# Kernel tuning notes

Measured on AMD Instinct MI355X. Metric: run time of the kernel, lower is better.

## Reference

```python
import jax, jax.numpy as jnp
import numpy as np

N = 20000
E = 320000
F_IN = 512
F_OUT = 512
DIFF_T = 1.0
NUM_STEPS = 5
TIME_DECAY = 0.1
LN_EPS = 1e-5


def setup_inputs() -> dict:
    key = jax.random.key(0)
    k_x, k_e, k_ts, k_wt, k_wr = jax.random.split(key, 5)
    x = jax.random.normal(k_x, (N, F_IN), dtype=jnp.float32)
    edge_index = jax.random.randint(k_e, (2, E), 0, N)
    timestamps = jax.random.uniform(k_ts, (E,), dtype=jnp.float32) * 100.0
    lim = float(np.sqrt(6.0 / (F_IN + F_OUT)))  # xavier_uniform
    W_t = jax.random.uniform(k_wt, (F_OUT, F_IN), jnp.float32, -lim, lim)
    b_t = jnp.zeros((F_OUT,), jnp.float32)
    W_r = jax.random.uniform(k_wr, (F_OUT, F_IN), jnp.float32, -lim, lim)
    gamma = jnp.ones((F_OUT,), jnp.float32)
    beta = jnp.zeros((F_OUT,), jnp.float32)
    return {"node_features": x, "edge_index": edge_index, "timestamps": timestamps,
            "W_t": W_t, "b_t": b_t, "W_r": W_r, "gamma": gamma, "beta": beta,
            "graph_time": 100}


def reference(node_features, edge_index, timestamps, W_t, b_t, W_r, gamma, beta, graph_time):
    x = node_features
    n = x.shape[0]
    # append self-loops with timestamp == graph.time
    loop = jnp.arange(n)
    ei = jnp.concatenate([edge_index, jnp.stack([loop, loop], axis=0)], axis=1)
    ts = jnp.concatenate([timestamps, jnp.full((n,), graph_time, jnp.float32)])
    src, dst = ei[0], ei[1]
    # time-decayed symmetric-normalized adjacency weights
    w = jnp.exp(-TIME_DECAY * (ts.max() - ts))  # [E+N]
    deg = jax.ops.segment_sum(w, dst, num_segments=n)  # [N]
    dinv = jnp.where(deg > 0, deg ** -0.5, 0.0)
    ew = dinv[src] * w * dinv[dst]  # [E+N]
    # K Euler steps of heat diffusion: h <- h + dt*(A_norm h - h)
    dt = DIFF_T / NUM_STEPS
    h = x
    for _ in range(NUM_STEPS):
        diffused = jax.ops.segment_sum(ew[:, None] * h[src], dst, num_segments=n)  # [N, F]
        h = h + dt * (diffused - h)
    # transform + residual + layernorm (dropout omitted: eval mode)
    out = jax.nn.relu(h @ W_t.T + b_t) + x @ W_r.T  # [N, F_OUT]
    mu = out.mean(axis=-1, keepdims=True)
    var = out.var(axis=-1, keepdims=True)
    out = (out - mu) * jax.lax.rsqrt(var + LN_EPS) * gamma + beta
    return out
```

## Files before the change

### kernel.cpp

```cpp
#include <hip/hip_runtime.h>
#include <hip/hip_fp16.h>

#define FDIM 512
#define TDK  0.1f
#define DTs  0.2f
#define EPSv 1e-5f

using bf16x8  = __attribute__((ext_vector_type(8))) __bf16;
using floatx4 = __attribute__((ext_vector_type(4))) float;
using ushort8 = __attribute__((ext_vector_type(8))) unsigned short;
using uintx4  = __attribute__((ext_vector_type(4))) unsigned int;

__device__ __forceinline__ unsigned short f2bf(float f) {
  unsigned int u = __float_as_uint(f);
  u += 0x7fffu + ((u >> 16) & 1u);
  return (unsigned short)(u >> 16);
}

__device__ __forceinline__ void gld16(const __bf16* g, __bf16* l) {
  __builtin_amdgcn_global_load_lds(
      (const __attribute__((address_space(1))) unsigned int*)g,
      (__attribute__((address_space(3))) unsigned int*)l, 16, 0, 0);
}

__global__ __launch_bounds__(256) void tsmax_kernel(const float* __restrict__ ts, int E,
                                                    float* __restrict__ out) {
  float m = 0.f;
  for (int i = blockIdx.x * blockDim.x + threadIdx.x; i < E; i += gridDim.x * blockDim.x)
    m = fmaxf(m, ts[i]);
  for (int off = 32; off; off >>= 1) m = fmaxf(m, __shfl_down(m, off));
  __shared__ float sm[4];
  int wid = threadIdx.x >> 6, lane = threadIdx.x & 63;
  if (lane == 0) sm[wid] = m;
  __syncthreads();
  if (threadIdx.x == 0) {
    float mm = fmaxf(fmaxf(sm[0], sm[1]), fmaxf(sm[2], sm[3]));
    atomicMax((int*)out, __float_as_int(mm));
  }
}

__global__ __launch_bounds__(256) void edge_w_deg(const int* __restrict__ src, const int* __restrict__ dst,
                                                  const float* __restrict__ ts, const float* __restrict__ tsmax_p,
                                                  const int* __restrict__ gt_p,
                                                  float* __restrict__ w, float* __restrict__ deg,
                                                  int* __restrict__ cnt, int E, int N) {
  int e = blockIdx.x * blockDim.x + threadIdx.x;
  int total = E + N;
  if (e >= total) return;
  float gtf = (float)(*gt_p);
  float tm = fmaxf(*tsmax_p, gtf);
  int d; float t;
  if (e < E) { d = dst[e]; t = ts[e]; }
  else       { d = e - E;  t = gtf; }
  float wv = expf(-TDK * (tm - t));
  w[e] = wv;
  atomicAdd(&deg[d], wv);
  atomicAdd(&cnt[d], 1);
}

__global__ __launch_bounds__(256) void dinv_kernel(const float* __restrict__ deg, float* __restrict__ dinv, int N) {
  int i = blockIdx.x * blockDim.x + threadIdx.x;
  if (i >= N) return;
  float d = deg[i];
  dinv[i] = (d > 0.f) ? rsqrtf(d) : 0.f;
}

__global__ __launch_bounds__(256) void seg_reduce(const int* __restrict__ cnt, int* __restrict__ bsum, int n) {
  int i = blockIdx.x * 256 + threadIdx.x;
  int v = (i < n) ? cnt[i] : 0;
  for (int o = 32; o; o >>= 1) v += __shfl_down(v, o);
  __shared__ int sm[4];
  if ((threadIdx.x & 63) == 0) sm[threadIdx.x >> 6] = v;
  __syncthreads();
  if (threadIdx.x == 0) bsum[blockIdx.x] = sm[0] + sm[1] + sm[2] + sm[3];
}

__global__ __launch_bounds__(256) void scan_bsum(const int* __restrict__ bsum, int* __restrict__ bbase, int nb) {
  __shared__ int sm[256];
  int t = threadIdx.x;
  int v = (t < nb) ? bsum[t] : 0;
  sm[t] = v;
  __syncthreads();
  for (int o = 1; o < 256; o <<= 1) {
    int u = (t >= o) ? sm[t - o] : 0;
    __syncthreads();
    sm[t] += u;
    __syncthreads();
  }
  if (t < nb) bbase[t] = sm[t] - v;
}

__global__ __launch_bounds__(256) void seg_scan(const int* __restrict__ cnt, const int* __restrict__ bbase,
                                                int* __restrict__ offs, int* __restrict__ cursor,
                                                int n, int totE) {
  __shared__ int sm[256];
  int i = blockIdx.x * 256 + threadIdx.x;
  int v = (i < n) ? cnt[i] : 0;
  sm[threadIdx.x] = v;
  __syncthreads();
  for (int o = 1; o < 256; o <<= 1) {
    int u = (threadIdx.x >= o) ? sm[threadIdx.x - o] : 0;
    __syncthreads();
    sm[threadIdx.x] += u;
    __syncthreads();
  }
  int excl = sm[threadIdx.x] - v + bbase[blockIdx.x];
  if (i < n) { offs[i] = excl; cursor[i] = excl; }
  if (i == 0) offs[n] = totE;
}

__global__ __launch_bounds__(256) void scatter_kernel(const int* __restrict__ src, const int* __restrict__ dst,
                                                      const float* __restrict__ w, const float* __restrict__ dinv,
                                                      int* __restrict__ cursor, unsigned* __restrict__ cv,
                                                      int E, int N) {
  int e = blockIdx.x * blockDim.x + threadIdx.x;
  if (e >= E + N) return;
  int s, d;
  if (e < E) { s = src[e]; d = dst[e]; }
  else       { s = d = e - E; }
  int pos = atomicAdd(&cursor[d], 1);
  float v = dinv[s] * w[e] * dinv[d];
  unsigned short hv = __half_as_ushort(__float2half(v));
  cv[pos] = (unsigned)s | ((unsigned)hv << 16);
}

__device__ __forceinline__ void acc8(uintx4 u, float v, float* a) {
  a[0] += v * __uint_as_float(u[0] << 16);
  a[1] += v * __uint_as_float(u[0] & 0xffff0000u);
  a[2] += v * __uint_as_float(u[1] << 16);
  a[3] += v * __uint_as_float(u[1] & 0xffff0000u);
  a[4] += v * __uint_as_float(u[2] << 16);
  a[5] += v * __uint_as_float(u[2] & 0xffff0000u);
  a[6] += v * __uint_as_float(u[3] << 16);
  a[7] += v * __uint_as_float(u[3] & 0xffff0000u);
}

__device__ __forceinline__ float cvval(unsigned cu) {
  return __half2float(__ushort_as_half((unsigned short)(cu >> 16)));
}

__global__ __launch_bounds__(256) void spmm_xcd(const int* __restrict__ offs, const unsigned* __restrict__ cv,
                                                const unsigned short* __restrict__ h_in,
                                                unsigned short* __restrict__ h_out, int N) {
  int chunk = blockIdx.x & 7;
  int tile  = blockIdx.x >> 3;
  int row = tile * 32 + (threadIdx.x >> 3);
  if (row >= N) return;
  int fo = chunk * 64 + (threadIdx.x & 7) * 8;
  const unsigned short* hp = h_in + fo;
  int s = offs[row], e = offs[row + 1];
  float a[8] = {0.f, 0.f, 0.f, 0.f, 0.f, 0.f, 0.f, 0.f};
  int j = s;
  for (; j + 8 <= e; j += 8) {
    unsigned cu[8]; uintx4 u[8];
#pragma unroll
    for (int t = 0; t < 8; ++t) cu[t] = cv[j + t];
#pragma unroll
    for (int t = 0; t < 8; ++t) u[t] = *(const uintx4*)(hp + ((cu[t] & 0xffffu) << 9));
#pragma unroll
    for (int t = 0; t < 8; ++t) acc8(u[t], cvval(cu[t]), a);
  }
  if (j + 4 <= e) {
    unsigned cu[4]; uintx4 u[4];
#pragma unroll
    for (int t = 0; t < 4; ++t) cu[t] = cv[j + t];
#pragma unroll
    for (int t = 0; t < 4; ++t) u[t] = *(const uintx4*)(hp + ((cu[t] & 0xffffu) << 9));
#pragma unroll
    for (int t = 0; t < 4; ++t) acc8(u[t], cvval(cu[t]), a);
    j += 4;
  }
  for (; j < e; ++j) {
    unsigned cu = cv[j];
    uintx4 u = *(const uintx4*)(hp + ((cu & 0xffffu) << 9));
    acc8(u, cvval(cu), a);
  }
  uintx4 ud = *(const uintx4*)(hp + (row << 9));
  float hd[8];
  hd[0] = __uint_as_float(ud[0] << 16); hd[1] = __uint_as_float(ud[0] & 0xffff0000u);
  hd[2] = __uint_as_float(ud[1] << 16); hd[3] = __uint_as_float(ud[1] & 0xffff0000u);
  hd[4] = __uint_as_float(ud[2] << 16); hd[5] = __uint_as_float(ud[2] & 0xffff0000u);
  hd[6] = __uint_as_float(ud[3] << 16); hd[7] = __uint_as_float(ud[3] & 0xffff0000u);
  uintx4 o;
  unsigned int p0, p1;
#define PACK(k0, k1, dst_)                                        \
  { float o0 = hd[k0] + DTs * (a[k0] - hd[k0]);                   \
    float o1 = hd[k1] + DTs * (a[k1] - hd[k1]);                   \
    p0 = f2bf(o0); p1 = f2bf(o1); dst_ = p0 | (p1 << 16); }
  PACK(0, 1, o[0]) PACK(2, 3, o[1]) PACK(4, 5, o[2]) PACK(6, 7, o[3])
#undef PACK
  __builtin_nontemporal_store(o, (uintx4*)(h_out + (size_t)row * FDIM + fo));
}

__global__ __launch_bounds__(256) void cast_bf16(const float* __restrict__ srcp,
                                                 unsigned short* __restrict__ dstp, int n8) {
  int i = blockIdx.x * blockDim.x + threadIdx.x;
  if (i >= n8) return;
  const float4 v0 = *(const float4*)(srcp + (size_t)i * 8);
  const float4 v1 = *(const float4*)(srcp + (size_t)i * 8 + 4);
  ushort8 o;
  o[0] = f2bf(v0.x); o[1] = f2bf(v0.y); o[2] = f2bf(v0.z); o[3] = f2bf(v0.w);
  o[4] = f2bf(v1.x); o[5] = f2bf(v1.y); o[6] = f2bf(v1.z); o[7] = f2bf(v1.w);
  *(ushort8*)(dstp + (size_t)i * 8) = o;
}

__global__ __launch_bounds__(256, 2) void gemm_fused(const __bf16* __restrict__ Ah, const __bf16* __restrict__ Ax,
                                                     const __bf16* __restrict__ Wt, const __bf16* __restrict__ Wr,
                                                     const float* __restrict__ bias, float* __restrict__ out,
                                                     int M) {
  __shared__ __bf16 sA1[2][128 * 32];
  __shared__ __bf16 sA2[2][128 * 32];
  __shared__ __bf16 sB1[2][128 * 32];
  __shared__ __bf16 sB2[2][128 * 32];
  int tid = threadIdx.x;
  int wid = tid >> 6, lane = tid & 63;
  int wm = wid & 1, wn = wid >> 1;
  int lane15 = lane & 15, quad = lane >> 4;
  int m0 = blockIdx.x * 128, n0 = blockIdx.y * 128;

  int r0 = wid * 32 + (lane >> 2);
  int c0 = ((((lane & 3) - (lane >> 3)) & 3)) * 8;
  int am0 = m0 + r0;      if (am0 >= M) am0 = M - 1;
  int am1 = m0 + r0 + 16; if (am1 >= M) am1 = M - 1;
  int bn0 = n0 + r0;
  const __bf16* gA1_0 = Ah + (size_t)am0 * FDIM + c0;
  const __bf16* gA1_1 = Ah + (size_t)am1 * FDIM + c0;
  const __bf16* gA2_0 = Ax + (size_t)am0 * FDIM + c0;
  const __bf16* gA2_1 = Ax + (size_t)am1 * FDIM + c0;
  const __bf16* gB1_0 = Wt + (size_t)bn0 * FDIM + c0;
  const __bf16* gB1_1 = Wt + (size_t)(bn0 + 16) * FDIM + c0;
  const __bf16* gB2_0 = Wr + (size_t)bn0 * FDIM + c0;
  const __bf16* gB2_1 = Wr + (size_t)(bn0 + 16) * FDIM + c0;
  int loff0 = wid * 1024;
  int loff1 = wid * 1024 + 512;

  auto stage = [&](int b, int kt) {
    gld16(gA1_0 + kt, &sA1[b][loff0]); gld16(gA1_1 + kt, &sA1[b][loff1]);
    gld16(gB1_0 + kt, &sB1[b][loff0]); gld16(gB1_1 + kt, &sB1[b][loff1]);
    gld16(gA2_0 + kt, &sA2[b][loff0]); gld16(gA2_1 + kt, &sA2[b][loff1]);
    gld16(gB2_0 + kt, &sB2[b][loff0]); gld16(gB2_1 + kt, &sB2[b][loff1]);
  };

  int koff = ((quad + (lane15 >> 1)) & 3) * 8;

  floatx4 acc1[4][4], acc2[4][4];
  floatx4 z4; z4[0] = 0.f; z4[1] = 0.f; z4[2] = 0.f; z4[3] = 0.f;
#pragma unroll
  for (int im = 0; im < 4; ++im)
#pragma unroll
    for (int in = 0; in < 4; ++in) { acc1[im][in] = z4; acc2[im][in] = z4; }

  stage(0, 0);
  for (int it = 0; it < 16; ++it) {
    int cb = it & 1;
    __syncthreads();
    if (it + 1 < 16) stage(1 - cb, (it + 1) * 32);
    bf16x8 af[4], br[4];
#pragma unroll
    for (int im = 0; im < 4; ++im)
      af[im] = *(const bf16x8*)(&sA1[cb][(wm * 64 + im * 16 + lane15) * 32 + koff]);
#pragma unroll
    for (int in = 0; in < 4; ++in)
      br[in] = *(const bf16x8*)(&sB1[cb][(wn * 64 + in * 16 + lane15) * 32 + koff]);
#pragma unroll
    for (int im = 0; im < 4; ++im)
#pragma unroll
      for (int in = 0; in < 4; ++in)
        acc1[im][in] = __builtin_amdgcn_mfma_f32_16x16x32_bf16(af[im], br[in], acc1[im][in], 0, 0, 0);
#pragma unroll
    for (int im = 0; im < 4; ++im)
      af[im] = *(const bf16x8*)(&sA2[cb][(wm * 64 + im * 16 + lane15) * 32 + koff]);
#pragma unroll
    for (int in = 0; in < 4; ++in)
      br[in] = *(const bf16x8*)(&sB2[cb][(wn * 64 + in * 16 + lane15) * 32 + koff]);
#pragma unroll
    for (int im = 0; im < 4; ++im)
#pragma unroll
      for (int in = 0; in < 4; ++in)
        acc2[im][in] = __builtin_amdgcn_mfma_f32_16x16x32_bf16(af[im], br[in], acc2[im][in], 0, 0, 0);
  }

  float bn[4];
#pragma unroll
  for (int in = 0; in < 4; ++in) bn[in] = bias[n0 + wn * 64 + in * 16 + lane15];
#pragma unroll
  for (int im = 0; im < 4; ++im) {
#pragma unroll
    for (int in = 0; in < 4; ++in) {
#pragma unroll
      for (int r = 0; r < 4; ++r) {
        int m = m0 + wm * 64 + im * 16 + quad * 4 + r;
        int n = n0 + wn * 64 + in * 16 + lane15;
        if (m < M) {
          float v = fmaxf(acc1[im][in][r] + bn[in], 0.f) + acc2[im][in][r];
          out[(size_t)m * FDIM + n] = v;
        }
      }
    }
  }
}

__global__ __launch_bounds__(256) void ln_kernel(const float* __restrict__ pre, const float* __restrict__ gamma,
                                                 const float* __restrict__ beta, float* __restrict__ out) {
  int row = blockIdx.x, t = threadIdx.x;
  float2 v = *(const float2*)(pre + (size_t)row * FDIM + t * 2);
  float s = v.x + v.y;
  float ss = v.x * v.x + v.y * v.y;
  for (int off = 32; off; off >>= 1) { s += __shfl_down(s, off); ss += __shfl_down(ss, off); }
  __shared__ float sm[4], sm2[4];
  int wid = t >> 6, lane = t & 63;
  if (lane == 0) { sm[wid] = s; sm2[wid] = ss; }
  __syncthreads();
  if (t == 0) {
    float a = sm[0] + sm[1] + sm[2] + sm[3];
    float b = sm2[0] + sm2[1] + sm2[2] + sm2[3];
    sm[0] = a; sm2[0] = b;
  }
  __syncthreads();
  float mu = sm[0] * (1.f / FDIM);
  float var = sm2[0] * (1.f / FDIM) - mu * mu;
  float inv = rsqrtf(var + EPSv);
  float2 g  = *(const float2*)(gamma + t * 2);
  float2 bb = *(const float2*)(beta + t * 2);
  float2 o;
  o.x = (v.x - mu) * inv * g.x + bb.x;
  o.y = (v.y - mu) * inv * g.y + bb.y;
  *(float2*)(out + (size_t)row * FDIM + t * 2) = o;
}

extern "C" void kernel_launch(void* const* d_in, const int* in_sizes, int n_in,
                              void* d_out, int out_size, void* d_ws, size_t ws_size,
                              hipStream_t stream) {
  const float* x     = (const float*)d_in[0];
  const int*   ei    = (const int*)d_in[1];
  const float* ts    = (const float*)d_in[2];
  const float* W_t   = (const float*)d_in[3];
  const float* b_t   = (const float*)d_in[4];
  const float* W_r   = (const float*)d_in[5];
  const float* gamma = (const float*)d_in[6];
  const float* beta  = (const float*)d_in[7];
  const int*   gt    = (const int*)d_in[8];

  const int E = in_sizes[2];
  const int N = in_sizes[0] / FDIM;
  const int* src = ei;
  const int* dst = ei + E;
  const int totE = E + N;
  const int nb = (N + 255) / 256;

  char* base = (char*)d_ws;
  size_t off = 0;
  auto carve = [&](size_t bytes) -> char* {
    char* r = base + off;
    off = (off + bytes + 255) & ~(size_t)255;
    return r;
  };
  float* tsmax = (float*)carve(4);
  float* deg   = (float*)carve((size_t)N * 4);
  int*   cnt   = (int*)  carve((size_t)N * 4);
  size_t zero_bytes = off;
  float* dinv  = (float*)carve((size_t)N * 4);
  int*   offs  = (int*)  carve((size_t)(N + 1) * 4);
  int*   cursor= (int*)  carve((size_t)N * 4);
  int*   bsum  = (int*)  carve((size_t)nb * 4);
  int*   bbase = (int*)  carve((size_t)nb * 4);
  float* w     = (float*)carve((size_t)totE * 4);
  unsigned* cv = (unsigned*)carve((size_t)totE * 4);
  unsigned short* xb  = (unsigned short*)carve((size_t)N * FDIM * 2);
  unsigned short* hba = (unsigned short*)carve((size_t)N * FDIM * 2);
  unsigned short* hbb = (unsigned short*)carve((size_t)N * FDIM * 2);
  unsigned short* wtb = (unsigned short*)carve((size_t)FDIM * FDIM * 2);
  unsigned short* wrb = (unsigned short*)carve((size_t)FDIM * FDIM * 2);
  float* preLN = (float*)carve((size_t)N * FDIM * 4);

  hipMemsetAsync(d_ws, 0, zero_bytes, stream);

  tsmax_kernel<<<64, 256, 0, stream>>>(ts, E, tsmax);
  edge_w_deg<<<(totE + 255) / 256, 256, 0, stream>>>(src, dst, ts, tsmax, gt, w, deg, cnt, E, N);
  dinv_kernel<<<(N + 255) / 256, 256, 0, stream>>>(deg, dinv, N);
  seg_reduce<<<nb, 256, 0, stream>>>(cnt, bsum, N);
  scan_bsum<<<1, 256, 0, stream>>>(bsum, bbase, nb);
  seg_scan<<<nb, 256, 0, stream>>>(cnt, bbase, offs, cursor, N, totE);
  scatter_kernel<<<(totE + 255) / 256, 256, 0, stream>>>(src, dst, w, dinv, cursor, cv, E, N);

  int n8x = N * FDIM / 8;
  cast_bf16<<<(n8x + 255) / 256, 256, 0, stream>>>(x, xb, n8x);
  int n8w = FDIM * FDIM / 8;
  cast_bf16<<<(n8w + 255) / 256, 256, 0, stream>>>(W_t, wtb, n8w);
  cast_bf16<<<(n8w + 255) / 256, 256, 0, stream>>>(W_r, wrb, n8w);

  int sgrid = ((N + 31) / 32) * 8;
  spmm_xcd<<<sgrid, 256, 0, stream>>>(offs, cv, xb,  hba, N);
  spmm_xcd<<<sgrid, 256, 0, stream>>>(offs, cv, hba, hbb, N);
  spmm_xcd<<<sgrid, 256, 0, stream>>>(offs, cv, hbb, hba, N);
  spmm_xcd<<<sgrid, 256, 0, stream>>>(offs, cv, hba, hbb, N);
  spmm_xcd<<<sgrid, 256, 0, stream>>>(offs, cv, hbb, hba, N);

  dim3 gg((N + 127) / 128, FDIM / 128);
  gemm_fused<<<gg, 256, 0, stream>>>((const __bf16*)hba, (const __bf16*)xb,
                                     (const __bf16*)wtb, (const __bf16*)wrb,
                                     b_t, preLN, N);

  ln_kernel<<<N, 256, 0, stream>>>(preLN, gamma, beta, (float*)d_out);
}
```

Baseline: 403.1 us.

## Serialize dual GEMM into one accumulator and remap blocks per XCD

The fused GEMM now computes relu(h·W_tᵀ+b) first into a single accumulator set over 16 k-steps, applies bias and ReLU in place, then keeps accumulating x·W_rᵀ over another 16 steps. This halves the accumulator registers and the shared-memory tiles so three blocks per CU can fit. Block indices are also remapped to a 1D grid so that consecutive tiles land on the same XCD, improving L2 reuse of A rows. The cost is a serialized 32-step loop with the same MFMA count and one extra branch per iteration.

```diff
diff --git a/kernel.cpp b/kernel.cpp
--- a/kernel.cpp
+++ b/kernel.cpp
@@ -204,97 +204,100 @@
   *(ushort8*)(dstp + (size_t)i * 8) = o;
 }
 
-__global__ __launch_bounds__(256, 2) void gemm_fused(const __bf16* __restrict__ Ah, const __bf16* __restrict__ Ax,
+__global__ __launch_bounds__(256, 3) void gemm_fused(const __bf16* __restrict__ Ah, const __bf16* __restrict__ Ax,
                                                      const __bf16* __restrict__ Wt, const __bf16* __restrict__ Wr,
                                                      const float* __restrict__ bias, float* __restrict__ out,
-                                                     int M) {
-  __shared__ __bf16 sA1[2][128 * 32];
-  __shared__ __bf16 sA2[2][128 * 32];
-  __shared__ __bf16 sB1[2][128 * 32];
-  __shared__ __bf16 sB2[2][128 * 32];
+                                                     int M, int NB) {
+  __shared__ __bf16 sA[2][128 * 32];
+  __shared__ __bf16 sB[2][128 * 32];
   int tid = threadIdx.x;
   int wid = tid >> 6, lane = tid & 63;
   int wm = wid & 1, wn = wid >> 1;
   int lane15 = lane & 15, quad = lane >> 4;
-  int m0 = blockIdx.x * 128, n0 = blockIdx.y * 128;
+
+  int d = blockIdx.x;
+  int x = d & 7, s = d >> 3;
+  int q = NB >> 3, r = NB & 7;
+  int g = (x < r ? x * (q + 1) : r * (q + 1) + (x - r) * q) + s;
+  int mi = g >> 2, ni = g & 3;
+  int m0 = mi * 128, n0 = ni * 128;
 
   int r0 = wid * 32 + (lane >> 2);
   int c0 = ((((lane & 3) - (lane >> 3)) & 3)) * 8;
   int am0 = m0 + r0;      if (am0 >= M) am0 = M - 1;
   int am1 = m0 + r0 + 16; if (am1 >= M) am1 = M - 1;
   int bn0 = n0 + r0;
-  const __bf16* gA1_0 = Ah + (size_t)am0 * FDIM + c0;
-  const __bf16* gA1_1 = Ah + (size_t)am1 * FDIM + c0;
-  const __bf16* gA2_0 = Ax + (size_t)am0 * FDIM + c0;
-  const __bf16* gA2_1 = Ax + (size_t)am1 * FDIM + c0;
-  const __bf16* gB1_0 = Wt + (size_t)bn0 * FDIM + c0;
-  const __bf16* gB1_1 = Wt + (size_t)(bn0 + 16) * FDIM + c0;
-  const __bf16* gB2_0 = Wr + (size_t)bn0 * FDIM + c0;
-  const __bf16* gB2_1 = Wr + (size_t)(bn0 + 16) * FDIM + c0;
+  const __bf16* a00 = Ah + (size_t)am0 * FDIM + c0;
+  const __bf16* a01 = Ah + (size_t)am1 * FDIM + c0;
+  const __bf16* a10 = Ax + (size_t)am0 * FDIM + c0;
+  const __bf16* a11 = Ax + (size_t)am1 * FDIM + c0;
+  const __bf16* b00 = Wt + (size_t)bn0 * FDIM + c0;
+  const __bf16* b01 = Wt + (size_t)(bn0 + 16) * FDIM + c0;
+  const __bf16* b10 = Wr + (size_t)bn0 * FDIM + c0;
+  const __bf16* b11 = Wr + (size_t)(bn0 + 16) * FDIM + c0;
   int loff0 = wid * 1024;
   int loff1 = wid * 1024 + 512;
 
-  auto stage = [&](int b, int kt) {
-    gld16(gA1_0 + kt, &sA1[b][loff0]); gld16(gA1_1 + kt, &sA1[b][loff1]);
-    gld16(gB1_0 + kt, &sB1[b][loff0]); gld16(gB1_1 + kt, &sB1[b][loff1]);
-    gld16(gA2_0 + kt, &sA2[b][loff0]); gld16(gA2_1 + kt, &sA2[b][loff1]);
-    gld16(gB2_0 + kt, &sB2[b][loff0]); gld16(gB2_1 + kt, &sB2[b][loff1]);
+  auto stage = [&](int b, const __bf16* pa0, const __bf16* pa1,
+                   const __bf16* pb0, const __bf16* pb1, int kt) {
+    gld16(pa0 + kt, &sA[b][loff0]); gld16(pa1 + kt, &sA[b][loff1]);
+    gld16(pb0 + kt, &sB[b][loff0]); gld16(pb1 + kt, &sB[b][loff1]);
   };
 
   int koff = ((quad + (lane15 >> 1)) & 3) * 8;
 
-  floatx4 acc1[4][4], acc2[4][4];
+  float bn[4];
+#pragma unroll
+  for (int in = 0; in < 4; ++in) bn[in] = bias[n0 + wn * 64 + in * 16 + lane15];
+
+  floatx4 acc[4][4];
   floatx4 z4; z4[0] = 0.f; z4[1] = 0.f; z4[2] = 0.f; z4[3] = 0.f;
 #pragma unroll
   for (int im = 0; im < 4; ++im)
 #pragma unroll
-    for (int in = 0; in < 4; ++in) { acc1[im][in] = z4; acc2[im][in] = z4; }
-
-  stage(0, 0);
-  for (int it = 0; it < 16; ++it) {
+    for (int in = 0; in < 4; ++in) acc[im][in] = z4;
+
+  stage(0, a00, a01, b00, b01, 0);
+  for (int it = 0; it < 32; ++it) {
     int cb = it & 1;
     __syncthreads();
-    if (it + 1 < 16) stage(1 - cb, (it + 1) * 32);
+    int nx = it + 1;
+    if (nx < 32) {
+      if (nx < 16) stage(1 - cb, a00, a01, b00, b01, nx * 32);
+      else         stage(1 - cb, a10, a11, b10, b11, (nx & 15) * 32);
+    }
+    if (it == 16) {
+#pragma unroll
+      for (int im = 0; im < 4; ++im)
+#pragma unroll
+        for (int in = 0; in < 4; ++in)
+#pragma unroll
+          for (int rr = 0; rr < 4; ++rr)
+            acc[im][in][rr] = fmaxf(acc[im][in][rr] + bn[in], 0.f);
+    }
     bf16x8 af[4], br[4];
 #pragma unroll
     for (int im = 0; im < 4; ++im)
-      af[im] = *(const bf16x8*)(&sA1[cb][(wm * 64 + im * 16 + lane15) * 32 + koff]);
+      af[im] = *(const bf16x8*)(&sA[cb][(wm * 64 + im * 16 + lane15) * 32 + koff]);
 #pragma unroll
     for (int in = 0; in < 4; ++in)
-      br[in] = *(const bf16x8*)(&sB1[cb][(wn * 64 + in * 16 + lane15) * 32 + koff]);
+      br[in] = *(const bf16x8*)(&sB[cb][(wn * 64 + in * 16 + lane15) * 32 + koff]);
 #pragma unroll
     for (int im = 0; im < 4; ++im)
 #pragma unroll
       for (int in = 0; in < 4; ++in)
-        acc1[im][in] = __builtin_amdgcn_mfma_f32_16x16x32_bf16(af[im], br[in], acc1[im][in], 0, 0, 0);
-#pragma unroll
-    for (int im = 0; im < 4; ++im)
-      af[im] = *(const bf16x8*)(&sA2[cb][(wm * 64 + im * 16 + lane15) * 32 + koff]);
-#pragma unroll
-    for (int in = 0; in < 4; ++in)
-      br[in] = *(const bf16x8*)(&sB2[cb][(wn * 64 + in * 16 + lane15) * 32 + koff]);
-#pragma unroll
-    for (int im = 0; im < 4; ++im)
-#pragma unroll
-      for (int in = 0; in < 4; ++in)
-        acc2[im][in] = __builtin_amdgcn_mfma_f32_16x16x32_bf16(af[im], br[in], acc2[im][in], 0, 0, 0);
-  }
-
-  float bn[4];
-#pragma unroll
-  for (int in = 0; in < 4; ++in) bn[in] = bias[n0 + wn * 64 + in * 16 + lane15];
+        acc[im][in] = __builtin_amdgcn_mfma_f32_16x16x32_bf16(af[im], br[in], acc[im][in], 0, 0, 0);
+  }
+
 #pragma unroll
   for (int im = 0; im < 4; ++im) {
 #pragma unroll
     for (int in = 0; in < 4; ++in) {
 #pragma unroll
-      for (int r = 0; r < 4; ++r) {
-        int m = m0 + wm * 64 + im * 16 + quad * 4 + r;
+      for (int rr = 0; rr < 4; ++rr) {
+        int m = m0 + wm * 64 + im * 16 + quad * 4 + rr;
         int n = n0 + wn * 64 + in * 16 + lane15;
-        if (m < M) {
-          float v = fmaxf(acc1[im][in][r] + bn[in], 0.f) + acc2[im][in][r];
-          out[(size_t)m * FDIM + n] = v;
-        }
+        if (m < M) out[(size_t)m * FDIM + n] = acc[im][in][rr];
       }
     }
   }
@@ -396,10 +399,11 @@
   spmm_xcd<<<sgrid, 256, 0, stream>>>(offs, cv, hba, hbb, N);
   spmm_xcd<<<sgrid, 256, 0, stream>>>(offs, cv, hbb, hba, N);
 
-  dim3 gg((N + 127) / 128, FDIM / 128);
-  gemm_fused<<<gg, 256, 0, stream>>>((const __bf16*)hba, (const __bf16*)xb,
-                                     (const __bf16*)wtb, (const __bf16*)wrb,
-                                     b_t, preLN, N);
+  int MB = (N + 127) / 128;
+  int NBLK = MB * (FDIM / 128);
+  gemm_fused<<<NBLK, 256, 0, stream>>>((const __bf16*)hba, (const __bf16*)xb,
+                                       (const __bf16*)wtb, (const __bf16*)wrb,
+                                       b_t, preLN, N, NBLK);
 
   ln_kernel<<<N, 256, 0, stream>>>(preLN, gamma, beta, (float*)d_out);
 }
```

Result: faster. 381.9 us (-5.3%).
